# Optimization experiments

Measured on AMD Instinct MI355X. Metric: run time of the kernel, lower is better.

## Reference

```python
import jax, jax.numpy as jnp
import numpy as np

N, D, K, P = 4096, 256, 16, 3
MAXDEG = K + 1          # self loop guarantees deg >= 1, randint caps deg <= K+1
TAU, LAM, BETA, MARGIN = 0.8, 0.5, 1.0, 0.1
EPS_PD = 1e-6           # F.pairwise_distance eps (added to the difference)


def _make_adj(k):
    nbr = jax.random.randint(k, (N, K), 0, N)
    m = jnp.zeros((N, N), jnp.float32)
    m = m.at[jnp.arange(N)[:, None], nbr].set(1.0)
    m = m.at[jnp.arange(N), jnp.arange(N)].set(1.0)
    return m / m.sum(1, keepdims=True)  # row-normalized metapath adjacency


def setup_inputs():
    key = jax.random.key(0)
    ks = jax.random.split(key, 12)
    g = 1.414 * (2.0 / (D + D)) ** 0.5  # xavier_normal gain=1.414
    return {
        "h": jax.random.normal(ks[0], (N, D), jnp.float32),
        "mps": jnp.stack([_make_adj(ks[1 + i]) for i in range(P)]),
        "W_gcn": jax.random.normal(ks[4], (P, D, D), jnp.float32) * g,
        "b_gcn": jnp.zeros((P, D), jnp.float32),
        "prelu_a": jnp.full((P,), 0.25, jnp.float32),
        "att_fc_W": jax.random.normal(ks[5], (D, D), jnp.float32) * g,
        "att_fc_b": jnp.zeros((D,), jnp.float32),
        "att_vec": jax.random.normal(ks[6], (D,), jnp.float32) * g,
        "proj_W1": jax.random.normal(ks[7], (D, D), jnp.float32) * g,
        "proj_b1": jnp.zeros((D,), jnp.float32),
        "proj_W2": jax.random.normal(ks[8], (D, D), jnp.float32) * g,
        "proj_b2": jnp.zeros((D,), jnp.float32),
    }


def _gcn(h, adj, W, b, a):
    out = adj @ (h @ W.T) + b          # spmm(adj, fc(h)) + bias
    return jnp.where(out > 0, out, a * out)  # PReLU


def _node_loss(emb, adj):
    # vectorized form of the per-node nonzero/pairwise_distance loop
    mask = adj > 0                      # [N, N]
    deg = mask.sum(1)                   # [N], >= 1 via self loops
    # stable argsort: neighbors first (ascending index), matching torch.nonzero order
    pos_idx = jnp.argsort(~mask, axis=1)[:, :MAXDEG]
    neg_idx = jnp.argsort(mask, axis=1)[:, :MAXDEG]   # first deg non-neighbors
    anc = emb[:, None, :]               # anchor expanded over pairs
    dp = jnp.sum((anc - emb[pos_idx] + EPS_PD) ** 2, -1)  # [N, MAXDEG]
    dn = jnp.sum((anc - emb[neg_idx] + EPS_PD) ** 2, -1)
    valid = jnp.arange(MAXDEG)[None, :] < deg[:, None]
    per = jnp.maximum(dp - dn + MARGIN, 0.0) * valid
    return jnp.sum(per.sum(1) / deg.astype(emb.dtype))  # per-node mean, summed


def _proj(z, W1, b1, W2, b2):
    return jax.nn.elu(z @ W1.T + b1) @ W2.T + b2


def _contrast(z1, z2, pos, W1, b1, W2, b2):
    p1 = _proj(z1, W1, b1, W2, b2)
    p2 = _proj(z2, W1, b1, W2, b2)
    n1 = jnp.linalg.norm(p1, axis=-1, keepdims=True)
    n2 = jnp.linalg.norm(p2, axis=-1, keepdims=True)
    sim = jnp.exp((p1 @ p2.T) / (n1 * n2.T) / TAU)     # [N, N]
    m12 = sim / (sim.sum(1, keepdims=True) + 1e-8)
    m21 = sim.T / (sim.T.sum(1, keepdims=True) + 1e-8)
    l12 = -jnp.log((m12 * pos).sum(-1)).mean()
    l21 = -jnp.log((m21 * pos).sum(-1)).mean()
    return LAM * l12 + (1.0 - LAM) * l21


def reference(h, mps, W_gcn, b_gcn, prelu_a, att_fc_W, att_fc_b, att_vec,
              proj_W1, proj_b1, proj_W2, proj_b2):
    embeds = [_gcn(h, mps[i], W_gcn[i], b_gcn[i], prelu_a[i]) for i in range(P)]
    node_loss = sum(_node_loss(embeds[i], mps[i]) for i in range(P))
    # faithful to original control flow: i==0 inner loop overwrites self.loss,
    # so only the (0, P-1) pair survives from i==0
    closs = _contrast(embeds[0], embeds[P - 1], mps[0], proj_W1, proj_b1, proj_W2, proj_b2)
    for i in range(1, P - 1):
        for j in range(i + 1, P):
            closs = closs + _contrast(embeds[i], embeds[j], mps[i], proj_W1, proj_b1, proj_W2, proj_b2)
    # semantic attention over metapaths
    sp = jnp.stack([jnp.tanh(e @ att_fc_W.T + att_fc_b).mean(0) for e in embeds])  # [P, D]
    beta = jax.nn.softmax(sp @ att_vec)                                            # [P]
    z_mp = jnp.einsum('p,pnd->nd', beta, jnp.stack(embeds))
    return z_mp, node_loss + BETA * closs
```

## Files before the change

### kernel.cpp

```cpp
#include <hip/hip_runtime.h>
#include <hip/hip_bf16.h>

constexpr int N = 4096;
constexpr int D = 256;
constexpr int P = 3;
constexpr int MAXDEG = 17;
constexpr float TAU = 0.8f;
constexpr float MARGIN = 0.1f;
constexpr float EPS_PD = 1e-6f;

constexpr int LDP = 40;

constexpr int OFF_H    = 0;
constexpr int OFF_WG   = 1048576;
constexpr int OFF_ATTW = 1245184;
constexpr int OFF_W1   = 1310720;
constexpr int OFF_W2   = 1376256;
constexpr int OFF_BG   = 1441792;
constexpr int OFF_ATTB = 1442560;
constexpr int OFF_AV   = 1442816;
constexpr int OFF_PA   = 1443072;
constexpr int OFF_B1   = 1443328;
constexpr int OFF_B2   = 1443584;
constexpr int CONV_TOTAL = 1443840;

typedef __attribute__((ext_vector_type(8))) short bfrag8;
typedef __attribute__((ext_vector_type(4))) float facc4;

__device__ inline facc4 mfma16(bfrag8 a, bfrag8 b, facc4 c) {
    return __builtin_amdgcn_mfma_f32_16x16x32_bf16(a, b, c, 0, 0, 0);
}
__device__ inline float b2f(__hip_bfloat16 v) { return __bfloat162float(v); }
__device__ inline float bfbits2f(unsigned short u) {
    return __uint_as_float(((unsigned int)u) << 16);
}

__device__ inline float load_in(const void* p, size_t i, int bf) {
    return bf ? __bfloat162float(((const __hip_bfloat16*)p)[i])
              : ((const float*)p)[i];
}

__global__ void detect_dtype(const unsigned int* __restrict__ w, int nwords,
                             int* __restrict__ counter) {
    int stride = gridDim.x * blockDim.x;
    int c = 0;
    for (int i = blockIdx.x * blockDim.x + threadIdx.x; i < nwords; i += stride) {
        unsigned int x = w[i];
        if ((x & 0xFFFF0000u) == 0u && x != 0u) c++;
    }
    for (int s = 32; s > 0; s >>= 1) c += __shfl_down(c, s);
    if ((threadIdx.x & 63) == 0 && c > 0) atomicAdd(counter, c);
}
__global__ void finalize_flag(const int* __restrict__ counter, int* __restrict__ flag) {
    flag[0] = (counter[0] > 100) ? 1 : 0;
}

__global__ void convert_all(const void* h, const void* wg, const void* attw,
                            const void* w1, const void* w2, const void* bg,
                            const void* attb, const void* av, const void* pa,
                            const void* b1, const void* b2,
                            const int* __restrict__ dflag,
                            __hip_bfloat16* __restrict__ dst) {
    int bf = dflag[0];
    const void* srcs[11] = {h, wg, attw, w1, w2, bg, attb, av, pa, b1, b2};
    const int offs[11] = {OFF_H, OFF_WG, OFF_ATTW, OFF_W1, OFF_W2, OFF_BG,
                          OFF_ATTB, OFF_AV, OFF_PA, OFF_B1, OFF_B2};
    const int lens[11] = {1048576, 196608, 65536, 65536, 65536, 768, 256, 256, 3, 256, 256};
    int stride = gridDim.x * blockDim.x;
    int t0 = blockIdx.x * blockDim.x + threadIdx.x;
    #pragma unroll
    for (int s = 0; s < 11; s++) {
        for (int i = t0; i < lens[s]; i += stride)
            dst[offs[s] + i] = __float2bfloat16(load_in(srcs[s], i, bf));
    }
}

__global__ void extract_sparse(const void* __restrict__ mps, const int* __restrict__ dflag,
                               int* __restrict__ nbr_idx, float* __restrict__ nbr_val,
                               int* __restrict__ neg_idx, int* __restrict__ deg) {
    int bf = dflag[0];
    int row = blockIdx.x;
    int t = threadIdx.x;
    __shared__ int cnt;
    __shared__ int sidx[32];
    __shared__ float sval[32];
    if (t == 0) cnt = 0;
    __syncthreads();
    int e0 = t * 16;
    if (bf) {
        const uint4* base = (const uint4*)((const __hip_bfloat16*)mps + (size_t)row * N + e0);
        #pragma unroll
        for (int v = 0; v < 2; v++) {
            uint4 w = base[v];
            unsigned int ws[4] = {w.x, w.y, w.z, w.w};
            #pragma unroll
            for (int j = 0; j < 4; j++) {
                unsigned short lo = (unsigned short)(ws[j] & 0xFFFFu);
                unsigned short hi = (unsigned short)(ws[j] >> 16);
                if (lo) { int k = atomicAdd(&cnt, 1); if (k < 32) { sidx[k] = e0 + v * 8 + j * 2;     sval[k] = bfbits2f(lo); } }
                if (hi) { int k = atomicAdd(&cnt, 1); if (k < 32) { sidx[k] = e0 + v * 8 + j * 2 + 1; sval[k] = bfbits2f(hi); } }
            }
        }
    } else {
        const float4* base = (const float4*)((const float*)mps + (size_t)row * N + e0);
        #pragma unroll
        for (int v = 0; v < 4; v++) {
            float4 w = base[v];
            float ws[4] = {w.x, w.y, w.z, w.w};
            #pragma unroll
            for (int j = 0; j < 4; j++)
                if (ws[j] > 0.f) { int k = atomicAdd(&cnt, 1); if (k < 32) { sidx[k] = e0 + v * 4 + j; sval[k] = ws[j]; } }
        }
    }
    __syncthreads();
    if (t == 0) {
        int dg = cnt; if (dg > MAXDEG) dg = MAXDEG;
        for (int i = 1; i < dg; i++) {
            int ki = sidx[i]; float kv = sval[i]; int j = i - 1;
            while (j >= 0 && sidx[j] > ki) { sidx[j+1] = sidx[j]; sval[j+1] = sval[j]; j--; }
            sidx[j+1] = ki; sval[j+1] = kv;
        }
        deg[row] = dg;
        int* oi = nbr_idx + (size_t)row * MAXDEG;
        float* ov = nbr_val + (size_t)row * MAXDEG;
        int* ng = neg_idx + (size_t)row * MAXDEG;
        for (int i = 0; i < MAXDEG; i++) { oi[i] = (i < dg) ? sidx[i] : 0; ov[i] = (i < dg) ? sval[i] : 0.f; }
        int c = 0, j = 0, found = 0;
        while (found < MAXDEG) {
            if (j < dg && sidx[j] == c) { j++; c++; continue; }
            ng[found++] = c++;
        }
    }
}

template <int ACT, bool WRITE, bool COLSUM>
__global__ void gemm_mfma(const __hip_bfloat16* __restrict__ Abase, size_t strideA,
                          const __hip_bfloat16* __restrict__ Bbase, size_t strideB,
                          const __hip_bfloat16* __restrict__ bias, size_t strideBias,
                          __hip_bfloat16* __restrict__ Cbase, size_t strideC,
                          float* __restrict__ csBase, size_t strideCS) {
    int z = blockIdx.z;
    const __hip_bfloat16* A = Abase + (size_t)z * strideA;
    const __hip_bfloat16* B = Bbase + (size_t)z * strideB;
    __shared__ __align__(16) __hip_bfloat16 As[64 * LDP];
    __shared__ __align__(16) __hip_bfloat16 Bs[64 * LDP];
    int bm = blockIdx.x * 64, bn = blockIdx.y * 64;
    int tid = threadIdx.x, wave = tid >> 6, lane = tid & 63;
    int quad = lane >> 4, l15 = lane & 15;
    int wr = (wave & 1) * 32, wc = (wave >> 1) * 32;
    facc4 acc[2][2] = {};
    int sr = tid >> 2, kq = (tid & 3) * 8;
    for (int k0 = 0; k0 < D; k0 += 32) {
        *(bfrag8*)&As[sr * LDP + kq] = *(const bfrag8*)&A[(size_t)(bm + sr) * D + k0 + kq];
        *(bfrag8*)&Bs[sr * LDP + kq] = *(const bfrag8*)&B[(size_t)(bn + sr) * D + k0 + kq];
        __syncthreads();
        bfrag8 af[2], bfr[2];
        #pragma unroll
        for (int mi = 0; mi < 2; mi++)
            af[mi] = *(const bfrag8*)&As[(wr + mi * 16 + l15) * LDP + quad * 8];
        #pragma unroll
        for (int ni = 0; ni < 2; ni++)
            bfr[ni] = *(const bfrag8*)&Bs[(wc + ni * 16 + l15) * LDP + quad * 8];
        #pragma unroll
        for (int mi = 0; mi < 2; mi++)
            #pragma unroll
            for (int ni = 0; ni < 2; ni++)
                acc[mi][ni] = mfma16(af[mi], bfr[ni], acc[mi][ni]);
        __syncthreads();
    }
    float cs[2] = {0.f, 0.f};
    #pragma unroll
    for (int mi = 0; mi < 2; mi++) {
        #pragma unroll
        for (int ni = 0; ni < 2; ni++) {
            int col = bn + wc + ni * 16 + l15;
            #pragma unroll
            for (int r = 0; r < 4; r++) {
                int row = bm + wr + mi * 16 + quad * 4 + r;
                float v = acc[mi][ni][r];
                if (bias) v += b2f(bias[(size_t)z * strideBias + col]);
                if (ACT == 1) v = v > 0.f ? v : expm1f(v);
                if (ACT == 2) v = tanhf(v);
                if (WRITE) Cbase[(size_t)z * strideC + (size_t)row * D + col] = __float2bfloat16(v);
                if (COLSUM) cs[ni] += v;
            }
        }
    }
    if (COLSUM) {
        #pragma unroll
        for (int ni = 0; ni < 2; ni++) {
            float v = cs[ni];
            v += __shfl_xor(v, 16); v += __shfl_xor(v, 32);
            if (quad == 0) {
                int col = bn + wc + ni * 16 + l15;
                atomicAdd(&csBase[(size_t)z * strideCS + col], v);
            }
        }
    }
}

__global__ void spmm_prelu(const __hip_bfloat16* __restrict__ Xbase,
                           const int* __restrict__ nbr_idx, const float* __restrict__ nbr_val,
                           const int* __restrict__ deg, const __hip_bfloat16* __restrict__ conv,
                           __hip_bfloat16* __restrict__ embBase) {
    int z = blockIdx.z, n = blockIdx.x, d = threadIdx.x;
    const __hip_bfloat16* X = Xbase + (size_t)z * N * D;
    const int* idx = nbr_idx + ((size_t)z * N + n) * MAXDEG;
    const float* val = nbr_val + ((size_t)z * N + n) * MAXDEG;
    int dg = deg[z * N + n];
    float acc = 0.f;
    for (int k = 0; k < dg; k++) acc += val[k] * b2f(X[(size_t)idx[k] * D + d]);
    acc += b2f(conv[OFF_BG + z * D + d]);
    float a = b2f(conv[OFF_PA + z]);
    embBase[(size_t)z * N * D + (size_t)n * D + d] = __float2bfloat16(acc > 0.f ? acc : a * acc);
}

__global__ void rownorm(__hip_bfloat16* __restrict__ qbase) {
    int z = blockIdx.z, n = blockIdx.x, t = threadIdx.x;
    __hip_bfloat16* row = qbase + ((size_t)z * N + n) * D;
    float v = b2f(row[t]);
    __shared__ float red[256];
    red[t] = v * v;
    __syncthreads();
    for (int s = 128; s > 0; s >>= 1) { if (t < s) red[t] += red[t + s]; __syncthreads(); }
    float inv = rsqrtf(red[0] + 1e-30f);
    row[t] = __float2bfloat16(v * inv);
}

__global__ void sim_mfma(const __hip_bfloat16* __restrict__ q,
                         float* __restrict__ rowsum, float* __restrict__ colsum) {
    int pair = blockIdx.z;
    const __hip_bfloat16* Qa = q + (size_t)pair * N * D;
    const __hip_bfloat16* Qb = q + (size_t)2 * N * D;
    __shared__ __align__(16) __hip_bfloat16 As[128 * LDP];
    __shared__ __align__(16) __hip_bfloat16 Bs[128 * LDP];
    int bm = blockIdx.x * 128, bn = blockIdx.y * 128;
    int tid = threadIdx.x, wave = tid >> 6, lane = tid & 63;
    int quad = lane >> 4, l15 = lane & 15;
    int wr = (wave & 1) * 64, wc = (wave >> 1) * 64;
    facc4 acc[4][4] = {};
    int sr = tid >> 2, kq = (tid & 3) * 8;
    for (int k0 = 0; k0 < D; k0 += 32) {
        *(bfrag8*)&As[sr * LDP + kq]        = *(const bfrag8*)&Qa[(size_t)(bm + sr) * D + k0 + kq];
        *(bfrag8*)&As[(sr + 64) * LDP + kq] = *(const bfrag8*)&Qa[(size_t)(bm + sr + 64) * D + k0 + kq];
        *(bfrag8*)&Bs[sr * LDP + kq]        = *(const bfrag8*)&Qb[(size_t)(bn + sr) * D + k0 + kq];
        *(bfrag8*)&Bs[(sr + 64) * LDP + kq] = *(const bfrag8*)&Qb[(size_t)(bn + sr + 64) * D + k0 + kq];
        __syncthreads();
        bfrag8 af[4], bfr[4];
        #pragma unroll
        for (int mi = 0; mi < 4; mi++)
            af[mi] = *(const bfrag8*)&As[(wr + mi * 16 + l15) * LDP + quad * 8];
        #pragma unroll
        for (int ni = 0; ni < 4; ni++)
            bfr[ni] = *(const bfrag8*)&Bs[(wc + ni * 16 + l15) * LDP + quad * 8];
        #pragma unroll
        for (int mi = 0; mi < 4; mi++)
            #pragma unroll
            for (int ni = 0; ni < 4; ni++)
                acc[mi][ni] = mfma16(af[mi], bfr[ni], acc[mi][ni]);
        __syncthreads();
    }
    constexpr float invtau = 1.0f / TAU;
    float rs[4][4];
    float cs[4] = {0.f, 0.f, 0.f, 0.f};
    #pragma unroll
    for (int mi = 0; mi < 4; mi++)
        #pragma unroll
        for (int r = 0; r < 4; r++) rs[mi][r] = 0.f;
    #pragma unroll
    for (int mi = 0; mi < 4; mi++)
        #pragma unroll
        for (int ni = 0; ni < 4; ni++)
            #pragma unroll
            for (int r = 0; r < 4; r++) {
                float e = __expf(acc[mi][ni][r] * invtau);
                rs[mi][r] += e;
                cs[ni] += e;
            }
    #pragma unroll
    for (int mi = 0; mi < 4; mi++)
        #pragma unroll
        for (int r = 0; r < 4; r++) {
            float v = rs[mi][r];
            v += __shfl_xor(v, 1); v += __shfl_xor(v, 2);
            v += __shfl_xor(v, 4); v += __shfl_xor(v, 8);
            rs[mi][r] = v;
        }
    if (l15 == 0) {
        #pragma unroll
        for (int mi = 0; mi < 4; mi++)
            #pragma unroll
            for (int r = 0; r < 4; r++)
                atomicAdd(&rowsum[(size_t)pair * N + bm + wr + mi * 16 + quad * 4 + r], rs[mi][r]);
    }
    #pragma unroll
    for (int ni = 0; ni < 4; ni++) {
        float v = cs[ni];
        v += __shfl_xor(v, 16); v += __shfl_xor(v, 32);
        if (quad == 0)
            atomicAdd(&colsum[(size_t)pair * N + bn + wc + ni * 16 + l15], v);
    }
}

__global__ void posdot(const __hip_bfloat16* __restrict__ q,
                       const int* __restrict__ nbr_idx, const float* __restrict__ nbr_val,
                       const int* __restrict__ deg,
                       float* __restrict__ pdrow, float* __restrict__ pdcol) {
    int pair = blockIdx.z;
    int wave = threadIdx.x >> 6, lane = threadIdx.x & 63;
    int n = blockIdx.x * 4 + wave;
    const __hip_bfloat16* Qa = q + (size_t)pair * N * D;
    const __hip_bfloat16* Qb = q + (size_t)2 * N * D;
    int dg = deg[pair * N + n];
    const int* idx = nbr_idx + ((size_t)pair * N + n) * MAXDEG;
    const float* val = nbr_val + ((size_t)pair * N + n) * MAXDEG;
    const float invtau = 1.0f / TAU;
    ushort4 ar = *(const ushort4*)&Qa[(size_t)n * D + lane * 4];
    ushort4 br = *(const ushort4*)&Qb[(size_t)n * D + lane * 4];
    float a[4] = {bfbits2f(ar.x), bfbits2f(ar.y), bfbits2f(ar.z), bfbits2f(ar.w)};
    float b[4] = {bfbits2f(br.x), bfbits2f(br.y), bfbits2f(br.z), bfbits2f(br.w)};
    float sr = 0.f, sc = 0.f;
    for (int k = 0; k < dg; k++) {
        int j = idx[k];
        ushort4 pj = *(const ushort4*)&Qb[(size_t)j * D + lane * 4];
        ushort4 aj = *(const ushort4*)&Qa[(size_t)j * D + lane * 4];
        float dr = a[0] * bfbits2f(pj.x) + a[1] * bfbits2f(pj.y) +
                   a[2] * bfbits2f(pj.z) + a[3] * bfbits2f(pj.w);
        float dc = b[0] * bfbits2f(aj.x) + b[1] * bfbits2f(aj.y) +
                   b[2] * bfbits2f(aj.z) + b[3] * bfbits2f(aj.w);
        #pragma unroll
        for (int s = 1; s <= 32; s <<= 1) { dr += __shfl_xor(dr, s); dc += __shfl_xor(dc, s); }
        sr += __expf(dr * invtau) * val[k];
        sc += __expf(dc * invtau) * val[k];
    }
    if (lane == 0) { pdrow[pair * N + n] = sr; pdcol[pair * N + n] = sc; }
}

__global__ void node_loss_k(const __hip_bfloat16* __restrict__ embBase,
                            const int* __restrict__ nbr_idx, const int* __restrict__ neg_idx,
                            const int* __restrict__ deg, float* __restrict__ nlpart) {
    int z = blockIdx.z;
    int wave = threadIdx.x >> 6, lane = threadIdx.x & 63;
    int n = blockIdx.x * 4 + wave;
    const __hip_bfloat16* emb = embBase + (size_t)z * N * D;
    int dg = deg[z * N + n];
    const int* ip = nbr_idx + ((size_t)z * N + n) * MAXDEG;
    const int* ig = neg_idx + ((size_t)z * N + n) * MAXDEG;
    ushort4 ar = *(const ushort4*)&emb[(size_t)n * D + lane * 4];
    float a[4] = {bfbits2f(ar.x), bfbits2f(ar.y), bfbits2f(ar.z), bfbits2f(ar.w)};
    float s = 0.f;
    for (int k = 0; k < dg; k++) {
        int jp = ip[k], jn = ig[k];
        ushort4 pr = *(const ushort4*)&emb[(size_t)jp * D + lane * 4];
        ushort4 nr = *(const ushort4*)&emb[(size_t)jn * D + lane * 4];
        float pv[4] = {bfbits2f(pr.x), bfbits2f(pr.y), bfbits2f(pr.z), bfbits2f(pr.w)};
        float nv[4] = {bfbits2f(nr.x), bfbits2f(nr.y), bfbits2f(nr.z), bfbits2f(nr.w)};
        float dp = 0.f, dn = 0.f;
        #pragma unroll
        for (int i = 0; i < 4; i++) {
            float x = a[i] - pv[i] + EPS_PD; dp += x * x;
            float y = a[i] - nv[i] + EPS_PD; dn += y * y;
        }
        #pragma unroll
        for (int st = 1; st <= 32; st <<= 1) { dp += __shfl_xor(dp, st); dn += __shfl_xor(dn, st); }
        float v = dp - dn + MARGIN;
        s += v > 0.f ? v : 0.f;
    }
    if (lane == 0) nlpart[z * N + n] = s / (float)dg;
}

__global__ void reduce_loss(const float* __restrict__ nlpart,
                            const float* __restrict__ rowsum, const float* __restrict__ colsum,
                            const float* __restrict__ pdrow, const float* __restrict__ pdcol,
                            float* __restrict__ loss) {
    int t = threadIdx.x;
    float s = 0.f;
    for (int i = t; i < P * N; i += 256) s += nlpart[i];
    for (int i = t; i < 2 * N; i += 256) {
        float l12 = -logf(pdrow[i] / (rowsum[i] + 1e-8f));
        float l21 = -logf(pdcol[i] / (colsum[i] + 1e-8f));
        s += (0.5f * l12 + 0.5f * l21) / (float)N;
    }
    __shared__ float red[256];
    red[t] = s;
    __syncthreads();
    for (int st = 128; st > 0; st >>= 1) { if (t < st) red[t] += red[t + st]; __syncthreads(); }
    if (t == 0) loss[0] = red[0];
}

__global__ void beta_k(const float* __restrict__ spacc, const __hip_bfloat16* __restrict__ conv,
                       float* __restrict__ beta) {
    __shared__ float red[256];
    __shared__ float w[P];
    int t = threadIdx.x;
    for (int p = 0; p < P; p++) {
        float v = (spacc[p * D + t] / (float)N) * b2f(conv[OFF_AV + t]);
        red[t] = v;
        __syncthreads();
        for (int s = 128; s > 0; s >>= 1) { if (t < s) red[t] += red[t + s]; __syncthreads(); }
        if (t == 0) w[p] = red[0];
        __syncthreads();
    }
    if (t == 0) {
        float m = fmaxf(w[0], fmaxf(w[1], w[2]));
        float e0 = __expf(w[0] - m), e1 = __expf(w[1] - m), e2 = __expf(w[2] - m);
        float s = e0 + e1 + e2;
        beta[0] = e0 / s; beta[1] = e1 / s; beta[2] = e2 / s;
    }
}

__global__ void zmp_out(const __hip_bfloat16* __restrict__ embBase, const float* __restrict__ beta,
                        const float* __restrict__ loss, const int* __restrict__ dflag,
                        void* __restrict__ out) {
    int bf = dflag[0];
    int i = blockIdx.x * 256 + threadIdx.x;
    float v = beta[0] * b2f(embBase[i]) + beta[1] * b2f(embBase[(size_t)N * D + i]) +
              beta[2] * b2f(embBase[(size_t)2 * N * D + i]);
    if (bf) {
        __hip_bfloat16* o = (__hip_bfloat16*)out;
        o[i] = __float2bfloat16(v);
        if (i == 0) o[(size_t)N * D] = __float2bfloat16(*loss);
    } else {
        float* o = (float*)out;
        o[i] = v;
        if (i == 0) o[(size_t)N * D] = *loss;
    }
}

extern "C" void kernel_launch(void* const* d_in, const int* in_sizes, int n_in,
                              void* d_out, int out_size, void* d_ws, size_t ws_size,
                              hipStream_t stream) {
    const void* h        = d_in[0];
    const void* mps      = d_in[1];
    const void* W_gcn    = d_in[2];
    const void* b_gcn    = d_in[3];
    const void* prelu_a  = d_in[4];
    const void* att_fc_W = d_in[5];
    const void* att_fc_b = d_in[6];
    const void* att_vec  = d_in[7];
    const void* proj_W1  = d_in[8];
    const void* proj_b1  = d_in[9];
    const void* proj_W2  = d_in[10];
    const void* proj_b2  = d_in[11];

    char* ws = (char*)d_ws;
    size_t off = 0;
    auto alloc = [&](size_t bytes) -> char* {
        char* p = ws + off;
        off = (off + bytes + 255) & ~(size_t)255;
        return p;
    };
    __hip_bfloat16* conv = (__hip_bfloat16*)alloc((size_t)CONV_TOTAL * 2);
    __hip_bfloat16* xbuf = (__hip_bfloat16*)alloc((size_t)P * N * D * 2);
    __hip_bfloat16* emb  = (__hip_bfloat16*)alloc((size_t)P * N * D * 2);
    __hip_bfloat16* q    = (__hip_bfloat16*)alloc((size_t)P * N * D * 2);
    int*   nbr_idx = (int*)alloc((size_t)P * N * MAXDEG * 4);
    float* nbr_val = (float*)alloc((size_t)P * N * MAXDEG * 4);
    int*   neg_idx = (int*)alloc((size_t)P * N * MAXDEG * 4);
    int*   deg     = (int*)alloc((size_t)P * N * 4);
    float* nlpart  = (float*)alloc((size_t)P * N * 4);
    float* pdrow   = (float*)alloc((size_t)2 * N * 4);
    float* pdcol   = (float*)alloc((size_t)2 * N * 4);
    char* zero_begin = ws + off;
    float* rowsum = (float*)alloc((size_t)2 * N * 4);
    float* colsum = (float*)alloc((size_t)2 * N * 4);
    float* spacc  = (float*)alloc((size_t)P * D * 4);
    float* beta   = (float*)alloc(16);
    float* loss   = (float*)alloc(16);
    int*   counter = (int*)alloc(16);
    int*   dflag   = (int*)alloc(16);
    size_t zero_bytes = (size_t)((ws + off) - zero_begin);
    hipMemsetAsync(zero_begin, 0, zero_bytes, stream);

    detect_dtype<<<1024, 256, 0, stream>>>((const unsigned int*)mps, 2 * 1024 * 1024, counter);
    finalize_flag<<<1, 1, 0, stream>>>(counter, dflag);

    convert_all<<<512, 256, 0, stream>>>(h, W_gcn, att_fc_W, proj_W1, proj_W2, b_gcn,
                                         att_fc_b, att_vec, prelu_a, proj_b1, proj_b2,
                                         dflag, conv);

    extract_sparse<<<P * N, 256, 0, stream>>>(mps, dflag, nbr_idx, nbr_val, neg_idx, deg);

    dim3 ggrid(N / 64, D / 64, P);
    size_t nd = (size_t)N * D;
    gemm_mfma<0, true, false><<<ggrid, 256, 0, stream>>>(
        conv + OFF_H, 0, conv + OFF_WG, (size_t)D * D, nullptr, 0, xbuf, nd, nullptr, 0);
    spmm_prelu<<<dim3(N, 1, P), 256, 0, stream>>>(xbuf, nbr_idx, nbr_val, deg, conv, emb);
    gemm_mfma<2, false, true><<<ggrid, 256, 0, stream>>>(
        emb, nd, conv + OFF_ATTW, 0, conv + OFF_ATTB, 0, nullptr, 0, spacc, (size_t)D);
    gemm_mfma<1, true, false><<<ggrid, 256, 0, stream>>>(
        emb, nd, conv + OFF_W1, 0, conv + OFF_B1, 0, xbuf, nd, nullptr, 0);
    gemm_mfma<0, true, false><<<ggrid, 256, 0, stream>>>(
        xbuf, nd, conv + OFF_W2, 0, conv + OFF_B2, 0, q, nd, nullptr, 0);
    rownorm<<<dim3(N, 1, P), 256, 0, stream>>>(q);
    sim_mfma<<<dim3(N / 128, N / 128, 2), 256, 0, stream>>>(q, rowsum, colsum);
    posdot<<<dim3(N / 4, 1, 2), 256, 0, stream>>>(q, nbr_idx, nbr_val, deg, pdrow, pdcol);
    node_loss_k<<<dim3(N / 4, 1, P), 256, 0, stream>>>(emb, nbr_idx, neg_idx, deg, nlpart);
    reduce_loss<<<1, 256, 0, stream>>>(nlpart, rowsum, colsum, pdrow, pdcol, loss);
    beta_k<<<1, 256, 0, stream>>>(spacc, conv, beta);
    zmp_out<<<(N * D) / 256, 256, 0, stream>>>(emb, beta, loss, dflag, d_out);
}
```

Before: 542.7 us.

## Fuse attention and projection GEMMs, vectorize spmm/rownorm, widen sim K-tile, merge small kernels

Two GEMMs that both read the embeddings (attention tanh colsum and projection ELU) become one dual GEMM that loads the A tile once. spmm_prelu and rownorm now handle one row per wave with 4-wide vector loads, and rownorm reduces with shuffles instead of a shared-memory tree. sim_mfma moves to a 64-wide K tile with half as many barriers. The finalize_flag and beta kernels are folded into their consumers to cut launches. The dual GEMM holds twice the accumulators, which may lower occupancy.

```diff
diff --git a/kernel.cpp b/kernel.cpp
--- a/kernel.cpp
+++ b/kernel.cpp
@@ -10,6 +10,7 @@
 constexpr float EPS_PD = 1e-6f;
 
 constexpr int LDP = 40;
+constexpr int LDK = 72;
 
 constexpr int OFF_H    = 0;
 constexpr int OFF_WG   = 1048576;
@@ -34,6 +35,11 @@
 __device__ inline float bfbits2f(unsigned short u) {
     return __uint_as_float(((unsigned int)u) << 16);
 }
+__device__ inline unsigned short f2bfbits(float v) {
+    __hip_bfloat16 t = __float2bfloat16(v);
+    return *(unsigned short*)&t;
+}
+__device__ inline int get_bf(const int* __restrict__ counter) { return counter[0] > 100; }
 
 __device__ inline float load_in(const void* p, size_t i, int bf) {
     return bf ? __bfloat162float(((const __hip_bfloat16*)p)[i])
@@ -51,17 +57,14 @@
     for (int s = 32; s > 0; s >>= 1) c += __shfl_down(c, s);
     if ((threadIdx.x & 63) == 0 && c > 0) atomicAdd(counter, c);
 }
-__global__ void finalize_flag(const int* __restrict__ counter, int* __restrict__ flag) {
-    flag[0] = (counter[0] > 100) ? 1 : 0;
-}
 
 __global__ void convert_all(const void* h, const void* wg, const void* attw,
                             const void* w1, const void* w2, const void* bg,
                             const void* attb, const void* av, const void* pa,
                             const void* b1, const void* b2,
-                            const int* __restrict__ dflag,
+                            const int* __restrict__ counter,
                             __hip_bfloat16* __restrict__ dst) {
-    int bf = dflag[0];
+    int bf = get_bf(counter);
     const void* srcs[11] = {h, wg, attw, w1, w2, bg, attb, av, pa, b1, b2};
     const int offs[11] = {OFF_H, OFF_WG, OFF_ATTW, OFF_W1, OFF_W2, OFF_BG,
                           OFF_ATTB, OFF_AV, OFF_PA, OFF_B1, OFF_B2};
@@ -75,10 +78,10 @@
     }
 }
 
-__global__ void extract_sparse(const void* __restrict__ mps, const int* __restrict__ dflag,
+__global__ void extract_sparse(const void* __restrict__ mps, const int* __restrict__ counter,
                                int* __restrict__ nbr_idx, float* __restrict__ nbr_val,
                                int* __restrict__ neg_idx, int* __restrict__ deg) {
-    int bf = dflag[0];
+    int bf = get_bf(counter);
     int row = blockIdx.x;
     int t = threadIdx.x;
     __shared__ int cnt;
@@ -133,12 +136,11 @@
     }
 }
 
-template <int ACT, bool WRITE, bool COLSUM>
+template <int ACT>
 __global__ void gemm_mfma(const __hip_bfloat16* __restrict__ Abase, size_t strideA,
                           const __hip_bfloat16* __restrict__ Bbase, size_t strideB,
                           const __hip_bfloat16* __restrict__ bias, size_t strideBias,
-                          __hip_bfloat16* __restrict__ Cbase, size_t strideC,
-                          float* __restrict__ csBase, size_t strideCS) {
+                          __hip_bfloat16* __restrict__ Cbase, size_t strideC) {
     int z = blockIdx.z;
     const __hip_bfloat16* A = Abase + (size_t)z * strideA;
     const __hip_bfloat16* B = Bbase + (size_t)z * strideB;
@@ -168,7 +170,6 @@
                 acc[mi][ni] = mfma16(af[mi], bfr[ni], acc[mi][ni]);
         __syncthreads();
     }
-    float cs[2] = {0.f, 0.f};
     #pragma unroll
     for (int mi = 0; mi < 2; mi++) {
         #pragma unroll
@@ -178,23 +179,80 @@
             for (int r = 0; r < 4; r++) {
                 int row = bm + wr + mi * 16 + quad * 4 + r;
                 float v = acc[mi][ni][r];
-                if (bias) v += b2f(bias[(size_t)z * strideBias + col]);
+                if (bias) v += b2f(bias[col]);
                 if (ACT == 1) v = v > 0.f ? v : expm1f(v);
-                if (ACT == 2) v = tanhf(v);
-                if (WRITE) Cbase[(size_t)z * strideC + (size_t)row * D + col] = __float2bfloat16(v);
-                if (COLSUM) cs[ni] += v;
+                Cbase[(size_t)z * strideC + (size_t)row * D + col] = __float2bfloat16(v);
             }
         }
     }
-    if (COLSUM) {
+}
+
+__global__ void gemm_dual(const __hip_bfloat16* __restrict__ embBase,
+                          const __hip_bfloat16* __restrict__ conv,
+                          __hip_bfloat16* __restrict__ xbuf,
+                          float* __restrict__ spacc) {
+    int z = blockIdx.z;
+    const __hip_bfloat16* A = embBase + (size_t)z * N * D;
+    const __hip_bfloat16* Ba = conv + OFF_ATTW;
+    const __hip_bfloat16* Bw = conv + OFF_W1;
+    __shared__ __align__(16) __hip_bfloat16 As[64 * LDP];
+    __shared__ __align__(16) __hip_bfloat16 Bsa[64 * LDP];
+    __shared__ __align__(16) __hip_bfloat16 Bsw[64 * LDP];
+    int bm = blockIdx.x * 64, bn = blockIdx.y * 64;
+    int tid = threadIdx.x, wave = tid >> 6, lane = tid & 63;
+    int quad = lane >> 4, l15 = lane & 15;
+    int wr = (wave & 1) * 32, wc = (wave >> 1) * 32;
+    facc4 accA[2][2] = {};
+    facc4 accW[2][2] = {};
+    int sr = tid >> 2, kq = (tid & 3) * 8;
+    for (int k0 = 0; k0 < D; k0 += 32) {
+        *(bfrag8*)&As[sr * LDP + kq]  = *(const bfrag8*)&A[(size_t)(bm + sr) * D + k0 + kq];
+        *(bfrag8*)&Bsa[sr * LDP + kq] = *(const bfrag8*)&Ba[(size_t)(bn + sr) * D + k0 + kq];
+        *(bfrag8*)&Bsw[sr * LDP + kq] = *(const bfrag8*)&Bw[(size_t)(bn + sr) * D + k0 + kq];
+        __syncthreads();
+        bfrag8 af[2], ba[2], bw[2];
+        #pragma unroll
+        for (int mi = 0; mi < 2; mi++)
+            af[mi] = *(const bfrag8*)&As[(wr + mi * 16 + l15) * LDP + quad * 8];
         #pragma unroll
         for (int ni = 0; ni < 2; ni++) {
-            float v = cs[ni];
-            v += __shfl_xor(v, 16); v += __shfl_xor(v, 32);
-            if (quad == 0) {
-                int col = bn + wc + ni * 16 + l15;
-                atomicAdd(&csBase[(size_t)z * strideCS + col], v);
+            ba[ni] = *(const bfrag8*)&Bsa[(wc + ni * 16 + l15) * LDP + quad * 8];
+            bw[ni] = *(const bfrag8*)&Bsw[(wc + ni * 16 + l15) * LDP + quad * 8];
+        }
+        #pragma unroll
+        for (int mi = 0; mi < 2; mi++)
+            #pragma unroll
+            for (int ni = 0; ni < 2; ni++) {
+                accA[mi][ni] = mfma16(af[mi], ba[ni], accA[mi][ni]);
+                accW[mi][ni] = mfma16(af[mi], bw[ni], accW[mi][ni]);
             }
+        __syncthreads();
+    }
+    float cs[2] = {0.f, 0.f};
+    #pragma unroll
+    for (int mi = 0; mi < 2; mi++) {
+        #pragma unroll
+        for (int ni = 0; ni < 2; ni++) {
+            int col = bn + wc + ni * 16 + l15;
+            float battb = b2f(conv[OFF_ATTB + col]);
+            float bb1   = b2f(conv[OFF_B1 + col]);
+            #pragma unroll
+            for (int r = 0; r < 4; r++) {
+                int row = bm + wr + mi * 16 + quad * 4 + r;
+                cs[ni] += tanhf(accA[mi][ni][r] + battb);
+                float v = accW[mi][ni][r] + bb1;
+                v = v > 0.f ? v : expm1f(v);
+                xbuf[(size_t)z * N * D + (size_t)row * D + col] = __float2bfloat16(v);
+            }
+        }
+    }
+    #pragma unroll
+    for (int ni = 0; ni < 2; ni++) {
+        float v = cs[ni];
+        v += __shfl_xor(v, 16); v += __shfl_xor(v, 32);
+        if (quad == 0) {
+            int col = bn + wc + ni * 16 + l15;
+            atomicAdd(&spacc[(size_t)z * D + col], v);
         }
     }
 }
@@ -203,28 +261,47 @@
                            const int* __restrict__ nbr_idx, const float* __restrict__ nbr_val,
                            const int* __restrict__ deg, const __hip_bfloat16* __restrict__ conv,
                            __hip_bfloat16* __restrict__ embBase) {
-    int z = blockIdx.z, n = blockIdx.x, d = threadIdx.x;
+    int z = blockIdx.z;
+    int wave = threadIdx.x >> 6, lane = threadIdx.x & 63;
+    int n = blockIdx.x * 4 + wave;
     const __hip_bfloat16* X = Xbase + (size_t)z * N * D;
     const int* idx = nbr_idx + ((size_t)z * N + n) * MAXDEG;
     const float* val = nbr_val + ((size_t)z * N + n) * MAXDEG;
     int dg = deg[z * N + n];
-    float acc = 0.f;
-    for (int k = 0; k < dg; k++) acc += val[k] * b2f(X[(size_t)idx[k] * D + d]);
-    acc += b2f(conv[OFF_BG + z * D + d]);
+    float acc[4] = {0.f, 0.f, 0.f, 0.f};
+    for (int k = 0; k < dg; k++) {
+        int j = idx[k];
+        float vk = val[k];
+        ushort4 x = *(const ushort4*)&X[(size_t)j * D + lane * 4];
+        acc[0] += vk * bfbits2f(x.x); acc[1] += vk * bfbits2f(x.y);
+        acc[2] += vk * bfbits2f(x.z); acc[3] += vk * bfbits2f(x.w);
+    }
+    ushort4 bb = *(const ushort4*)&conv[OFF_BG + z * D + lane * 4];
+    float b[4] = {bfbits2f(bb.x), bfbits2f(bb.y), bfbits2f(bb.z), bfbits2f(bb.w)};
     float a = b2f(conv[OFF_PA + z]);
-    embBase[(size_t)z * N * D + (size_t)n * D + d] = __float2bfloat16(acc > 0.f ? acc : a * acc);
+    ushort4 o;
+    float v0 = acc[0] + b[0]; o.x = f2bfbits(v0 > 0.f ? v0 : a * v0);
+    float v1 = acc[1] + b[1]; o.y = f2bfbits(v1 > 0.f ? v1 : a * v1);
+    float v2 = acc[2] + b[2]; o.z = f2bfbits(v2 > 0.f ? v2 : a * v2);
+    float v3 = acc[3] + b[3]; o.w = f2bfbits(v3 > 0.f ? v3 : a * v3);
+    *(ushort4*)&embBase[(size_t)z * N * D + (size_t)n * D + lane * 4] = o;
 }
 
 __global__ void rownorm(__hip_bfloat16* __restrict__ qbase) {
-    int z = blockIdx.z, n = blockIdx.x, t = threadIdx.x;
+    int z = blockIdx.z;
+    int wave = threadIdx.x >> 6, lane = threadIdx.x & 63;
+    int n = blockIdx.x * 4 + wave;
     __hip_bfloat16* row = qbase + ((size_t)z * N + n) * D;
-    float v = b2f(row[t]);
-    __shared__ float red[256];
-    red[t] = v * v;
-    __syncthreads();
-    for (int s = 128; s > 0; s >>= 1) { if (t < s) red[t] += red[t + s]; __syncthreads(); }
-    float inv = rsqrtf(red[0] + 1e-30f);
-    row[t] = __float2bfloat16(v * inv);
+    ushort4 r = *(const ushort4*)&row[lane * 4];
+    float v[4] = {bfbits2f(r.x), bfbits2f(r.y), bfbits2f(r.z), bfbits2f(r.w)};
+    float ss = v[0] * v[0] + v[1] * v[1] + v[2] * v[2] + v[3] * v[3];
+    #pragma unroll
+    for (int s = 1; s <= 32; s <<= 1) ss += __shfl_xor(ss, s);
+    float inv = rsqrtf(ss + 1e-30f);
+    ushort4 o;
+    o.x = f2bfbits(v[0] * inv); o.y = f2bfbits(v[1] * inv);
+    o.z = f2bfbits(v[2] * inv); o.w = f2bfbits(v[3] * inv);
+    *(ushort4*)&row[lane * 4] = o;
 }
 
 __global__ void sim_mfma(const __hip_bfloat16* __restrict__ q,
@@ -232,32 +309,37 @@
     int pair = blockIdx.z;
     const __hip_bfloat16* Qa = q + (size_t)pair * N * D;
     const __hip_bfloat16* Qb = q + (size_t)2 * N * D;
-    __shared__ __align__(16) __hip_bfloat16 As[128 * LDP];
-    __shared__ __align__(16) __hip_bfloat16 Bs[128 * LDP];
+    __shared__ __align__(16) __hip_bfloat16 As[128 * LDK];
+    __shared__ __align__(16) __hip_bfloat16 Bs[128 * LDK];
     int bm = blockIdx.x * 128, bn = blockIdx.y * 128;
     int tid = threadIdx.x, wave = tid >> 6, lane = tid & 63;
     int quad = lane >> 4, l15 = lane & 15;
     int wr = (wave & 1) * 64, wc = (wave >> 1) * 64;
     facc4 acc[4][4] = {};
-    int sr = tid >> 2, kq = (tid & 3) * 8;
-    for (int k0 = 0; k0 < D; k0 += 32) {
-        *(bfrag8*)&As[sr * LDP + kq]        = *(const bfrag8*)&Qa[(size_t)(bm + sr) * D + k0 + kq];
-        *(bfrag8*)&As[(sr + 64) * LDP + kq] = *(const bfrag8*)&Qa[(size_t)(bm + sr + 64) * D + k0 + kq];
-        *(bfrag8*)&Bs[sr * LDP + kq]        = *(const bfrag8*)&Qb[(size_t)(bn + sr) * D + k0 + kq];
-        *(bfrag8*)&Bs[(sr + 64) * LDP + kq] = *(const bfrag8*)&Qb[(size_t)(bn + sr + 64) * D + k0 + kq];
-        __syncthreads();
-        bfrag8 af[4], bfr[4];
-        #pragma unroll
-        for (int mi = 0; mi < 4; mi++)
-            af[mi] = *(const bfrag8*)&As[(wr + mi * 16 + l15) * LDP + quad * 8];
-        #pragma unroll
-        for (int ni = 0; ni < 4; ni++)
-            bfr[ni] = *(const bfrag8*)&Bs[(wc + ni * 16 + l15) * LDP + quad * 8];
-        #pragma unroll
-        for (int mi = 0; mi < 4; mi++)
+    int sr0 = tid >> 3, kq = (tid & 7) * 8;
+    for (int k0 = 0; k0 < D; k0 += 64) {
+        #pragma unroll
+        for (int i = 0; i < 4; i++) {
+            int r = sr0 + 32 * i;
+            *(bfrag8*)&As[r * LDK + kq] = *(const bfrag8*)&Qa[(size_t)(bm + r) * D + k0 + kq];
+            *(bfrag8*)&Bs[r * LDK + kq] = *(const bfrag8*)&Qb[(size_t)(bn + r) * D + k0 + kq];
+        }
+        __syncthreads();
+        #pragma unroll
+        for (int kk = 0; kk < 64; kk += 32) {
+            bfrag8 af[4], bfr[4];
+            #pragma unroll
+            for (int mi = 0; mi < 4; mi++)
+                af[mi] = *(const bfrag8*)&As[(wr + mi * 16 + l15) * LDK + kk + quad * 8];
             #pragma unroll
             for (int ni = 0; ni < 4; ni++)
-                acc[mi][ni] = mfma16(af[mi], bfr[ni], acc[mi][ni]);
+                bfr[ni] = *(const bfrag8*)&Bs[(wc + ni * 16 + l15) * LDK + kk + quad * 8];
+            #pragma unroll
+            for (int mi = 0; mi < 4; mi++)
+                #pragma unroll
+                for (int ni = 0; ni < 4; ni++)
+                    acc[mi][ni] = mfma16(af[mi], bfr[ni], acc[mi][ni]);
+        }
         __syncthreads();
     }
     constexpr float invtau = 1.0f / TAU;
@@ -369,11 +451,23 @@
     if (lane == 0) nlpart[z * N + n] = s / (float)dg;
 }
 
-__global__ void reduce_loss(const float* __restrict__ nlpart,
-                            const float* __restrict__ rowsum, const float* __restrict__ colsum,
-                            const float* __restrict__ pdrow, const float* __restrict__ pdcol,
-                            float* __restrict__ loss) {
+__global__ void reduce_loss_beta(const float* __restrict__ nlpart,
+                                 const float* __restrict__ rowsum, const float* __restrict__ colsum,
+                                 const float* __restrict__ pdrow, const float* __restrict__ pdcol,
+                                 const float* __restrict__ spacc,
+                                 const __hip_bfloat16* __restrict__ conv,
+                                 float* __restrict__ beta, float* __restrict__ loss) {
     int t = threadIdx.x;
+    __shared__ float red[256];
+    __shared__ float w[P];
+    for (int p = 0; p < P; p++) {
+        float v = (spacc[p * D + t] / (float)N) * b2f(conv[OFF_AV + t]);
+        red[t] = v;
+        __syncthreads();
+        for (int s = 128; s > 0; s >>= 1) { if (t < s) red[t] += red[t + s]; __syncthreads(); }
+        if (t == 0) w[p] = red[0];
+        __syncthreads();
+    }
     float s = 0.f;
     for (int i = t; i < P * N; i += 256) s += nlpart[i];
     for (int i = t; i < 2 * N; i += 256) {
@@ -381,38 +475,22 @@
         float l21 = -logf(pdcol[i] / (colsum[i] + 1e-8f));
         s += (0.5f * l12 + 0.5f * l21) / (float)N;
     }
-    __shared__ float red[256];
     red[t] = s;
     __syncthreads();
     for (int st = 128; st > 0; st >>= 1) { if (t < st) red[t] += red[t + st]; __syncthreads(); }
-    if (t == 0) loss[0] = red[0];
-}
-
-__global__ void beta_k(const float* __restrict__ spacc, const __hip_bfloat16* __restrict__ conv,
-                       float* __restrict__ beta) {
-    __shared__ float red[256];
-    __shared__ float w[P];
-    int t = threadIdx.x;
-    for (int p = 0; p < P; p++) {
-        float v = (spacc[p * D + t] / (float)N) * b2f(conv[OFF_AV + t]);
-        red[t] = v;
-        __syncthreads();
-        for (int s = 128; s > 0; s >>= 1) { if (t < s) red[t] += red[t + s]; __syncthreads(); }
-        if (t == 0) w[p] = red[0];
-        __syncthreads();
-    }
     if (t == 0) {
+        loss[0] = red[0];
         float m = fmaxf(w[0], fmaxf(w[1], w[2]));
         float e0 = __expf(w[0] - m), e1 = __expf(w[1] - m), e2 = __expf(w[2] - m);
-        float s = e0 + e1 + e2;
-        beta[0] = e0 / s; beta[1] = e1 / s; beta[2] = e2 / s;
+        float ssum = e0 + e1 + e2;
+        beta[0] = e0 / ssum; beta[1] = e1 / ssum; beta[2] = e2 / ssum;
     }
 }
 
 __global__ void zmp_out(const __hip_bfloat16* __restrict__ embBase, const float* __restrict__ beta,
-                        const float* __restrict__ loss, const int* __restrict__ dflag,
+                        const float* __restrict__ loss, const int* __restrict__ counter,
                         void* __restrict__ out) {
-    int bf = dflag[0];
+    int bf = get_bf(counter);
     int i = blockIdx.x * 256 + threadIdx.x;
     float v = beta[0] * b2f(embBase[i]) + beta[1] * b2f(embBase[(size_t)N * D + i]) +
               beta[2] * b2f(embBase[(size_t)2 * N * D + i]);
@@ -468,35 +546,30 @@
     float* beta   = (float*)alloc(16);
     float* loss   = (float*)alloc(16);
     int*   counter = (int*)alloc(16);
-    int*   dflag   = (int*)alloc(16);
     size_t zero_bytes = (size_t)((ws + off) - zero_begin);
     hipMemsetAsync(zero_begin, 0, zero_bytes, stream);
 
     detect_dtype<<<1024, 256, 0, stream>>>((const unsigned int*)mps, 2 * 1024 * 1024, counter);
-    finalize_flag<<<1, 1, 0, stream>>>(counter, dflag);
 
     convert_all<<<512, 256, 0, stream>>>(h, W_gcn, att_fc_W, proj_W1, proj_W2, b_gcn,
                                          att_fc_b, att_vec, prelu_a, proj_b1, proj_b2,
-                                         dflag, conv);
-
-    extract_sparse<<<P * N, 256, 0, stream>>>(mps, dflag, nbr_idx, nbr_val, neg_idx, deg);
+                                         counter, conv);
+
+    extract_sparse<<<P * N, 256, 0, stream>>>(mps, counter, nbr_idx, nbr_val, neg_idx, deg);
 
     dim3 ggrid(N / 64, D / 64, P);
     size_t nd = (size_t)N * D;
-    gemm_mfma<0, true, false><<<ggrid, 256, 0, stream>>>(
-        conv + OFF_H, 0, conv + OFF_WG, (size_t)D * D, nullptr, 0, xbuf, nd, nullptr, 0);
-    spmm_prelu<<<dim3(N, 1, P), 256, 0, stream>>>(xbuf, nbr_idx, nbr_val, deg, conv, emb);
-    gemm_mfma<2, false, true><<<ggrid, 256, 0, stream>>>(
-        emb, nd, conv + OFF_ATTW, 0, conv + OFF_ATTB, 0, nullptr, 0, spacc, (size_t)D);
-    gemm_mfma<1, true, false><<<ggrid, 256, 0, stream>>>(
-        emb, nd, conv + OFF_W1, 0, conv + OFF_B1, 0, xbuf, nd, nullptr, 0);
-    gemm_mfma<0, true, false><<<ggrid, 256, 0, stream>>>(
-        xbuf, nd, conv + OFF_W2, 0, conv + OFF_B2, 0, q, nd, nullptr, 0);
-    rownorm<<<dim3(N, 1, P), 256, 0, stream>>>(q);
+    gemm_mfma<0><<<ggrid, 256, 0, stream>>>(
+        conv + OFF_H, 0, conv + OFF_WG, (size_t)D * D, nullptr, 0, xbuf, nd);
+    spmm_prelu<<<dim3(N / 4, 1, P), 256, 0, stream>>>(xbuf, nbr_idx, nbr_val, deg, conv, emb);
+    gemm_dual<<<ggrid, 256, 0, stream>>>(emb, conv, xbuf, spacc);
+    gemm_mfma<0><<<ggrid, 256, 0, stream>>>(
+        xbuf, nd, conv + OFF_W2, 0, conv + OFF_B2, 0, q, nd);
+    rownorm<<<dim3(N / 4, 1, P), 256, 0, stream>>>(q);
     sim_mfma<<<dim3(N / 128, N / 128, 2), 256, 0, stream>>>(q, rowsum, colsum);
     posdot<<<dim3(N / 4, 1, 2), 256, 0, stream>>>(q, nbr_idx, nbr_val, deg, pdrow, pdcol);
     node_loss_k<<<dim3(N / 4, 1, P), 256, 0, stream>>>(emb, nbr_idx, neg_idx, deg, nlpart);
-    reduce_loss<<<1, 256, 0, stream>>>(nlpart, rowsum, colsum, pdrow, pdcol, loss);
-    beta_k<<<1, 256, 0, stream>>>(spacc, conv, beta);
-    zmp_out<<<(N * D) / 256, 256, 0, stream>>>(emb, beta, loss, dflag, d_out);
-}
+    reduce_loss_beta<<<1, 256, 0, stream>>>(nlpart, rowsum, colsum, pdrow, pdcol,
+                                            spacc, conv, beta, loss);
+    zmp_out<<<(N * D) / 256, 256, 0, stream>>>(emb, beta, loss, counter, d_out);
+}
```

Measured after the change: 510.4 us. 1.06x faster.
